# Optimization experiments

Measured on AMD Instinct MI355X. Metric: run time of the kernel, lower is better.

The kernel has to match this reference:

```python
import jax, jax.numpy as jnp
import numpy as np

NUM_FREQ = 64
DIM_OUTPUT = 512
CONST_INV_SOFTMAX = 1e-05


def setup_inputs() -> dict:
    key = jax.random.key(0)
    k1, k2, k3 = jax.random.split(key, 3)
    dim_input = 1024
    L = NUM_FREQ + 1
    batch = jax.random.normal(k1, (16, 4096, dim_input), dtype=jnp.float32)
    # nn.Linear default init (~U[-1/sqrt(fan_in), 1/sqrt(fan_in)]) then divided by 100
    bound = 1.0 / np.sqrt(dim_input)
    W = jax.random.uniform(k2, (2 * L, dim_input), minval=-bound, maxval=bound, dtype=jnp.float32) / 100.0
    b = jax.random.uniform(k3, (2 * L,), minval=-bound, maxval=bound, dtype=jnp.float32) / 100.0
    return {"batch": batch, "W": W, "b": b}


def _autocorrelate(a):
    # a: [B, L] complex. r[k] = sum_j a[j+k] * conj(a[j]), k = 0..L-1.
    # Equivalent to the grouped conv1d in the original; computed via zero-padded FFT.
    L = a.shape[-1]
    X = jnp.fft.fft(a, n=2 * L, axis=-1)
    r = jnp.fft.ifft(X * jnp.conj(X), axis=-1)
    return r[:, :L]


def reference(batch, W, b):
    L = NUM_FREQ + 1
    shape_out = batch.shape[:-1] + (DIM_OUTPUT,)
    x = batch.reshape(-1, batch.shape[-1])              # [B, d_in]
    p = x @ W.T + b                                      # [B, 2L]
    a = jax.lax.complex(p[:, :L], p[:, L:])              # [B, L] complex64
    r = _autocorrelate(a)                                # [B, L] fourier coeffs
    c = r[:, 1:] / r[:, :1].real                         # normalized coeffs [B, F]
    # bin centerpoints on [-1, 1]
    edges = jnp.linspace(-1.0, 1.0, DIM_OUTPUT + 1)
    centers = (edges[:-1] + edges[1:]) / 2               # [D]
    freqs = jnp.pi * jnp.arange(1, L, dtype=jnp.float32) # [F]
    phase = centers[:, None] * freqs[None, :]            # [D, F]
    # Re( sum_f c[b,f] * exp(i*phase[d,f]) ) = c.re @ cos - c.im @ sin
    like = 0.5 + c.real @ jnp.cos(phase).T - c.imag @ jnp.sin(phase).T  # [B, D]
    dist = like / jnp.sum(like, axis=-1, keepdims=True)
    logits = jnp.log(dist + CONST_INV_SOFTMAX)
    return logits.reshape(shape_out)
```

## Files before the change

### kernel.cpp

```cpp
#include <hip/hip_runtime.h>
#include <hip/hip_bf16.h>
#include <math.h>

#define BDIM 1024
#define NP   130
#define LL   65
#define NPAD 144
#define KP2  160
#define DOUT 512

typedef __attribute__((ext_vector_type(4))) float f32x4;
typedef __attribute__((ext_vector_type(8))) __bf16 bf16x8;

__global__ void fill_wbf(const float* __restrict__ W, __bf16* __restrict__ Wbf) {
  int idx = blockIdx.x * 256 + threadIdx.x;
  int c = idx >> 10, k = idx & 1023;
  float v = (c < NP) ? W[c * BDIM + k] : 0.f;
  Wbf[idx] = (__bf16)v;
}

__global__ void fill_mt(__bf16* __restrict__ Mt) {
  int idx = blockIdx.x * 256 + threadIdx.x;
  int d = idx / 80, jj = idx - d * 80;
  __bf16* col0 = Mt + (size_t)(2 * d) * KP2;
  __bf16* col1 = Mt + (size_t)(2 * d + 1) * KP2;
  if (jj < LL) {
    double theta = M_PI * (-1.0 + (2.0 * (double)d + 1.0) / 512.0);
    double ph = (double)jj * theta;
    double s = sin(ph), c = cos(ph);
    col0[jj]      = (__bf16)(float)c;
    col1[jj]      = (__bf16)(float)s;
    col0[LL + jj] = (__bf16)(float)(-s);
    col1[LL + jj] = (__bf16)(float)c;
  } else {
    int k = NP + (jj - LL);
    col0[k] = (__bf16)0.f; col1[k] = (__bf16)0.f;
    k += 15;
    col0[k] = (__bf16)0.f; col1[k] = (__bf16)0.f;
  }
}

__global__ __launch_bounds__(256) void gemm1(
    const float* __restrict__ X, const __bf16* __restrict__ Wbf,
    const float* __restrict__ bias, __bf16* __restrict__ P,
    float* __restrict__ R0) {
  const int tid  = threadIdx.x;
  const int w    = tid >> 6;
  const int lane = tid & 63;
  const int l15  = lane & 15;
  const int quad = lane >> 4;
  const long rowbase = (long)blockIdx.x * 64 + w * 16;

  f32x4 acc[9];
#pragma unroll
  for (int j = 0; j < 9; j++) acc[j] = (f32x4){0.f, 0.f, 0.f, 0.f};

  const float*  xptr = X   + (rowbase + l15) * BDIM + quad * 8;
  const __bf16* wptr = Wbf + (long)l15 * BDIM + quad * 8;

  f32x4 x0 = *(const f32x4*)(xptr);
  f32x4 x1 = *(const f32x4*)(xptr + 4);

#pragma unroll 2
  for (int k0 = 0; k0 < BDIM; k0 += 32) {
    const int kn = (k0 + 32 < BDIM) ? (k0 + 32) : k0;
    f32x4 n0 = *(const f32x4*)(xptr + kn);
    f32x4 n1 = *(const f32x4*)(xptr + kn + 4);

    bf16x8 a;
    a[0] = (__bf16)x0[0]; a[1] = (__bf16)x0[1];
    a[2] = (__bf16)x0[2]; a[3] = (__bf16)x0[3];
    a[4] = (__bf16)x1[0]; a[5] = (__bf16)x1[1];
    a[6] = (__bf16)x1[2]; a[7] = (__bf16)x1[3];

#pragma unroll
    for (int j = 0; j < 9; j++) {
      bf16x8 b = *(const bf16x8*)(wptr + (long)j * 16 * BDIM + k0);
      acc[j] = __builtin_amdgcn_mfma_f32_16x16x32_bf16(a, b, acc[j], 0, 0, 0);
    }
    x0 = n0; x1 = n1;
  }

  float s[4] = {0.f, 0.f, 0.f, 0.f};

#pragma unroll
  for (int j = 0; j < 9; j++) {
    int c = j * 16 + l15;
    float bj = (c < NP) ? bias[c] : 0.f;
#pragma unroll
    for (int reg = 0; reg < 4; reg++) {
      long row = rowbase + quad * 4 + reg;
      float pv = acc[j][reg] + bj;
      if (c >= NP) pv = 0.f;
      P[row * KP2 + c] = (__bf16)pv;
      s[reg] = fmaf(pv, pv, s[reg]);
    }
  }
#pragma unroll
  for (int reg = 0; reg < 4; reg++) {
    long row = rowbase + quad * 4 + reg;
    P[row * KP2 + NPAD + l15] = (__bf16)0.f;
  }
#pragma unroll
  for (int reg = 0; reg < 4; reg++) {
    float v = s[reg];
    v += __shfl_xor(v, 1);
    v += __shfl_xor(v, 2);
    v += __shfl_xor(v, 4);
    v += __shfl_xor(v, 8);
    if (l15 == 0) {
      long row = rowbase + quad * 4 + reg;
      R0[row] = 1.0f / (512.0f * v);
    }
  }
}

__global__ __launch_bounds__(256) void gemm2(
    const __bf16* __restrict__ P, const __bf16* __restrict__ Mt,
    const float* __restrict__ R0, float* __restrict__ out) {
  const int tid  = threadIdx.x;
  const int w    = tid >> 6;
  const int wr   = w >> 1, wc = w & 1;
  const int lane = tid & 63;
  const int l15  = lane & 15;
  const int quad = lane >> 4;
  const long rowbase = (long)blockIdx.x * 128 + wr * 64;
  const int  colbase = blockIdx.y * 128 + wc * 64;

  f32x4 acc[4][4];
#pragma unroll
  for (int rt = 0; rt < 4; rt++)
#pragma unroll
    for (int ct = 0; ct < 4; ct++) acc[rt][ct] = (f32x4){0.f, 0.f, 0.f, 0.f};

  const __bf16* pptr = P  + (rowbase + l15) * KP2 + quad * 8;
  const __bf16* mptr = Mt + (long)(colbase + l15) * KP2 + quad * 8;

#pragma unroll
  for (int k0 = 0; k0 < KP2; k0 += 32) {
    bf16x8 a[4], b[4];
#pragma unroll
    for (int t = 0; t < 4; t++) a[t] = *(const bf16x8*)(pptr + (long)t * 16 * KP2 + k0);
#pragma unroll
    for (int t = 0; t < 4; t++) b[t] = *(const bf16x8*)(mptr + (long)t * 16 * KP2 + k0);
#pragma unroll
    for (int rt = 0; rt < 4; rt++)
#pragma unroll
      for (int ct = 0; ct < 4; ct++)
        acc[rt][ct] = __builtin_amdgcn_mfma_f32_16x16x32_bf16(a[rt], b[ct], acc[rt][ct], 0, 0, 0);
  }

  const int par = lane & 1;
  float inv[4][2];
#pragma unroll
  for (int rt = 0; rt < 4; rt++)
#pragma unroll
    for (int q = 0; q < 2; q++)
      inv[rt][q] = R0[rowbase + rt * 16 + quad * 4 + par * 2 + q];

#pragma unroll
  for (int rt = 0; rt < 4; rt++) {
#pragma unroll
    for (int ct = 0; ct < 4; ct++) {
      const int d = (colbase >> 1) + ct * 8 + (l15 >> 1);
      float t[4];
#pragma unroll
      for (int reg = 0; reg < 4; reg++) {
        float v = acc[rt][ct][reg];
        t[reg] = v * v;
        t[reg] += __shfl_xor(t[reg], 1);
      }
#pragma unroll
      for (int q = 0; q < 2; q++) {
        int reg = par * 2 + q;
        long row = rowbase + rt * 16 + quad * 4 + reg;
        out[row * DOUT + d] = __logf(fmaf(t[reg], inv[rt][q], 1e-5f));
      }
    }
  }
}

extern "C" void kernel_launch(void* const* d_in, const int* in_sizes, int n_in,
                              void* d_out, int out_size, void* d_ws, size_t ws_size,
                              hipStream_t stream) {
  const float* X    = (const float*)d_in[0];
  const float* W    = (const float*)d_in[1];
  const float* bias = (const float*)d_in[2];
  float* out = (float*)d_out;
  const int B = in_sizes[0] / BDIM;

  char* ws = (char*)d_ws;
  __bf16* P   = (__bf16*)ws;                         ws += (size_t)B * KP2 * 2;
  __bf16* Wbf = (__bf16*)ws;                         ws += (size_t)NPAD * BDIM * 2;
  __bf16* Mt  = (__bf16*)ws;                         ws += (size_t)BDIM * KP2 * 2;
  float*  R0  = (float*)ws;

  fill_wbf<<<(NPAD * BDIM) / 256, 256, 0, stream>>>(W, Wbf);
  fill_mt<<<(512 * 80) / 256, 256, 0, stream>>>(Mt);
  gemm1<<<B / 64, 256, 0, stream>>>(X, Wbf, bias, P, R0);
  gemm2<<<dim3(B / 128, 8), 256, 0, stream>>>(P, Mt, R0, out);
}
```

Measured before the change: 544.1 us.

## Stage gemm1 X and W tiles through swizzled double-buffered LDS with async loads

The first GEMM now copies each 64x32 fp32 tile of X and the 144x32 bf16 tile of W into shared memory with global_load_lds, double-buffering so the next k-tile is fetched while the current one feeds the MFMAs. Previously each lane read X and W straight from global memory with a strided pattern, and W was re-read by every wave. XOR swizzles on the chunk index are meant to avoid LDS bank conflicts on the fragment reads. Launch bounds now request 4 blocks per CU. In exchange it adds a barrier every k-step and relies on the async LDS loads being complete at that barrier.

Measured after the change: 491.0 us. 9.8% less time.

```diff
diff --git a/kernel.cpp b/kernel.cpp
--- a/kernel.cpp
+++ b/kernel.cpp
@@ -8,9 +8,16 @@
 #define NPAD 144
 #define KP2  160
 #define DOUT 512
+#define BK   32
 
 typedef __attribute__((ext_vector_type(4))) float f32x4;
 typedef __attribute__((ext_vector_type(8))) __bf16 bf16x8;
+
+__device__ __forceinline__ void gload_lds16(const void* g, void* l) {
+  __builtin_amdgcn_global_load_lds(
+      (const __attribute__((address_space(1))) void*)g,
+      (__attribute__((address_space(3))) void*)l, 16, 0, 0);
+}
 
 __global__ void fill_wbf(const float* __restrict__ W, __bf16* __restrict__ Wbf) {
   int idx = blockIdx.x * 256 + threadIdx.x;
@@ -40,7 +47,7 @@
   }
 }
 
-__global__ __launch_bounds__(256) void gemm1(
+__global__ __launch_bounds__(256, 4) void gemm1(
     const float* __restrict__ X, const __bf16* __restrict__ Wbf,
     const float* __restrict__ bias, __bf16* __restrict__ P,
     float* __restrict__ R0) {
@@ -49,36 +56,75 @@
   const int lane = tid & 63;
   const int l15  = lane & 15;
   const int quad = lane >> 4;
-  const long rowbase = (long)blockIdx.x * 64 + w * 16;
+  const long row0   = (long)blockIdx.x * 64;
+  const long rowbase = row0 + w * 16;
+
+  __shared__ __align__(16) char Asmem[2][64 * BK * 4];
+  __shared__ __align__(16) char Bsmem[2][NPAD * BK * 2];
+
+  auto stageA = [&](int buf, int k0) {
+#pragma unroll
+    for (int c = 0; c < 2; c++) {
+      int t   = c * 256 + tid;
+      int row = t >> 3, cs = t & 7;
+      int cg  = cs ^ (row & 7);
+      const char* g = (const char*)(X + (row0 + row) * BDIM + k0) + cg * 16;
+      gload_lds16(g, &Asmem[buf][t * 16]);
+    }
+  };
+  auto stageB = [&](int buf, int k0) {
+#pragma unroll
+    for (int c = 0; c < 2; c++) {
+      int t   = c * 256 + tid;
+      int row = t >> 2, cs = t & 3;
+      int cg  = cs ^ ((row >> 1) & 3);
+      const char* g = (const char*)(Wbf + (long)row * BDIM + k0) + cg * 16;
+      gload_lds16(g, &Bsmem[buf][t * 16]);
+    }
+    if (tid < 64) {
+      int t   = 512 + tid;
+      int row = t >> 2, cs = t & 3;
+      int cg  = cs ^ ((row >> 1) & 3);
+      const char* g = (const char*)(Wbf + (long)row * BDIM + k0) + cg * 16;
+      gload_lds16(g, &Bsmem[buf][t * 16]);
+    }
+  };
 
   f32x4 acc[9];
 #pragma unroll
   for (int j = 0; j < 9; j++) acc[j] = (f32x4){0.f, 0.f, 0.f, 0.f};
 
-  const float*  xptr = X   + (rowbase + l15) * BDIM + quad * 8;
-  const __bf16* wptr = Wbf + (long)l15 * BDIM + quad * 8;
-
-  f32x4 x0 = *(const f32x4*)(xptr);
-  f32x4 x1 = *(const f32x4*)(xptr + 4);
+  stageA(0, 0);
+  stageB(0, 0);
+  __syncthreads();
+
+  const int r  = w * 16 + l15;
+  const int s0 = (2 * quad) ^ (r & 7);
+  const int s1 = s0 ^ 1;
 
 #pragma unroll 2
-  for (int k0 = 0; k0 < BDIM; k0 += 32) {
-    const int kn = (k0 + 32 < BDIM) ? (k0 + 32) : k0;
-    f32x4 n0 = *(const f32x4*)(xptr + kn);
-    f32x4 n1 = *(const f32x4*)(xptr + kn + 4);
-
+  for (int k0 = 0; k0 < BDIM; k0 += BK) {
+    const int cur = (k0 >> 5) & 1;
+    if (k0 + BK < BDIM) { stageA(cur ^ 1, k0 + BK); stageB(cur ^ 1, k0 + BK); }
+
+    const char* ab = &Asmem[cur][0];
+    f32x4 x0 = *(const f32x4*)(ab + r * 128 + s0 * 16);
+    f32x4 x1 = *(const f32x4*)(ab + r * 128 + s1 * 16);
     bf16x8 a;
     a[0] = (__bf16)x0[0]; a[1] = (__bf16)x0[1];
     a[2] = (__bf16)x0[2]; a[3] = (__bf16)x0[3];
     a[4] = (__bf16)x1[0]; a[5] = (__bf16)x1[1];
     a[6] = (__bf16)x1[2]; a[7] = (__bf16)x1[3];
 
+    const char* bb = &Bsmem[cur][0];
 #pragma unroll
     for (int j = 0; j < 9; j++) {
-      bf16x8 b = *(const bf16x8*)(wptr + (long)j * 16 * BDIM + k0);
+      int jr = j * 16 + l15;
+      int s  = quad ^ ((jr >> 1) & 3);
+      bf16x8 b = *(const bf16x8*)(bb + jr * 64 + s * 16);
       acc[j] = __builtin_amdgcn_mfma_f32_16x16x32_bf16(a, b, acc[j], 0, 0, 0);
     }
-    x0 = n0; x1 = n1;
+    __syncthreads();
   }
 
   float s[4] = {0.f, 0.f, 0.f, 0.f};
```
